# Optimization experiments

Hardware: AMD Instinct MI355X
Metric: run time of the kernel (lower is better)

Reference implementation:

```python
import jax, jax.numpy as jnp
import numpy as np

ES = 256
NUM_SPECIES, NUM_ABILITIES, NUM_ITEMS, NUM_MOVES = 1026, 300, 500, 920
NUM_ITEM_EFFECTS, NUM_GENDERS, NUM_STATUS, NUM_VOLATILE_STATUS = 16, 3, 8, 105
B, N, F = 8192, 12, 42
# feature layout (flat int32 vector per entity)
(SPECIES, ABILITY, ITEM, ITEM_EFFECT, GENDER, STATUS, BEING_CALLED_BACK, TRAPPED,
 NEWLY_SWITCHED, TOXIC_TURNS, SLEEP_TURNS, FAINTED, ACTIVE, SIDE, LEVEL, HP, MAXHP) = range(17)
BOOST0, VOL0, MOVEID0, MOVEPP0 = 17, 24, 33, 37  # 7 boosts, 9 volatile words, 4 moves, 4 pp

DENSE_DIMS = [("hp", 10), ("level", 7), ("active", 2), ("onehot", 32), ("boosts", 7),
              ("volatiles", NUM_VOLATILE_STATUS), ("item", ES + NUM_ITEM_EFFECTS),
              ("side", 2), ("moves", ES + 6)]

def _bits(x, world_dim):
    # binary-scale embedding: bit decomposition of an int feature
    nb = (world_dim - 1).bit_length()
    mask = jnp.asarray(1 << np.arange(nb), dtype=jnp.int32)
    return ((x[..., None] & mask) != 0).astype(jnp.float32)

def setup_inputs() -> dict:
    key = jax.random.key(0)
    ks = jax.random.split(key, 32)
    s = 0.02
    inp = {"entities": jax.random.randint(ks[0], (B, N, F), 0, 2, dtype=jnp.int32)}
    inp["embed_species"] = jax.random.normal(ks[1], (NUM_SPECIES, ES), jnp.float32) * s
    inp["embed_ability"] = jax.random.normal(ks[2], (NUM_ABILITIES, ES), jnp.float32) * s
    inp["embed_item"] = jax.random.normal(ks[3], (NUM_ITEMS, ES), jnp.float32) * s
    inp["embed_moves"] = jax.random.normal(ks[4], (NUM_MOVES, ES), jnp.float32) * s
    for i, (name, din) in enumerate(DENSE_DIMS):
        inp[f"{name}_W"] = jax.random.normal(ks[5 + i], (din, ES), jnp.float32) * s
        inp[f"{name}_b"] = jnp.zeros((ES,), jnp.float32)
    return inp

def _forward(entities, embed_species, embed_ability, embed_item, embed_moves,
             hp_W, hp_b, level_W, level_b, active_W, active_b, onehot_W, onehot_b,
             boosts_W, boosts_b, volatiles_W, volatiles_b, item_W, item_b,
             side_W, side_b, moves_W, moves_b):
    e = entities
    oh = jax.nn.one_hot
    dense = lambda x, W, b: x @ W + b
    hp = e[..., HP].astype(jnp.float32)
    maxhp = jnp.clip(e[..., MAXHP], 1).astype(jnp.float32)
    hp_ratio = jnp.clip(hp / maxhp, 0.0, 1.0)                      # (B,N)
    hp_token = jnp.floor(1023.0 * hp_ratio).astype(jnp.int32)
    boolean_code = jnp.concatenate([
        hp_ratio[..., None], oh(e[..., GENDER], NUM_GENDERS), oh(e[..., STATUS], NUM_STATUS),
        oh(e[..., BEING_CALLED_BACK], 2), oh(e[..., TRAPPED], 2), oh(e[..., NEWLY_SWITCHED], 2),
        oh(e[..., TOXIC_TURNS], 8), oh(e[..., SLEEP_TURNS], 4), oh(e[..., FAINTED], 2)], axis=-1)  # (B,N,32)
    item_onehot = jnp.concatenate([embed_item[e[..., ITEM]], oh(e[..., ITEM_EFFECT], NUM_ITEM_EFFECTS)], axis=-1)
    boosts = e[..., BOOST0:VOL0].astype(jnp.float32) / 2.0          # (B,N,7)
    vol = e[..., VOL0:VOL0 + 9]
    vbits = (vol[..., None] & jnp.arange(16)) > 0                   # (B,N,9,16)
    vol_oh = vbits.reshape(*vol.shape[:-1], 144)[..., :NUM_VOLATILE_STATUS].astype(jnp.float32)
    moveset = jnp.concatenate([embed_moves[e[..., MOVEID0:MOVEPP0]],
                               _bits(e[..., MOVEPP0:MOVEPP0 + 4], 64)], axis=-1)  # (B,N,4,262)
    moves_out = jnp.einsum('bnmf,fd->bnd', moveset, moves_W) + 4.0 * moves_b      # sum of 4 Dense outputs
    emb = (dense(_bits(hp_token, 1024), hp_W, hp_b)
           + dense(_bits(e[..., LEVEL], 101), level_W, level_b)
           + dense(oh(e[..., ACTIVE], 2), active_W, active_b)
           + dense(boolean_code, onehot_W, onehot_b)
           + dense(boosts, boosts_W, boosts_b)
           + dense(vol_oh, volatiles_W, volatiles_b)
           + embed_species[e[..., SPECIES]]
           + embed_ability[e[..., ABILITY]]
           + dense(item_onehot, item_W, item_b)
           + dense(oh(e[..., SIDE], 2), side_W, side_b)
           + moves_out)
    return emb

def reference(entities, embed_species, embed_ability, embed_item, embed_moves,
              hp_W, hp_b, level_W, level_b, active_W, active_b, onehot_W, onehot_b,
              boosts_W, boosts_b, volatiles_W, volatiles_b, item_W, item_b,
              side_W, side_b, moves_W, moves_b):
    return _forward(entities, embed_species, embed_ability, embed_item, embed_moves,
                    hp_W, hp_b, level_W, level_b, active_W, active_b, onehot_W, onehot_b,
                    boosts_W, boosts_b, volatiles_W, volatiles_b, item_W, item_b,
                    side_W, side_b, moves_W, moves_b)
```

## Files before the change

kernel.cpp:

```cpp
#include <hip/hip_runtime.h>
#include <hip/hip_fp16.h>

#define ES 256
#define NFEAT 42
#define NENT (8192 * 12)

#define F_SPECIES 0
#define F_ABILITY 1
#define F_ITEM 2
#define F_ITEM_EFFECT 3
#define F_GENDER 4
#define F_STATUS 5
#define F_BCB 6
#define F_TRAPPED 7
#define F_NEWSW 8
#define F_TOXIC 9
#define F_SLEEP 10
#define F_FAINTED 11
#define F_ACTIVE 12
#define F_SIDE 13
#define F_LEVEL 14
#define F_HP 15
#define F_MAXHP 16
#define F_BOOST0 17
#define F_VOL0 24
#define F_MOVEID0 33
#define F_MOVEPP0 37

#define OFF_HP     0
#define OFF_LV     (OFF_HP + 1024*ES)
#define OFF_PP     (OFF_LV + 128*ES)
#define OFF_VP     (OFF_PP + 64*ES)
#define OFF_CA     (OFF_VP + 784*ES)
#define OFF_CB     (OFF_CA + 768*ES)
#define OFF_EI     (OFF_CB + 1024*ES)
#define OFF_EM     (OFF_EI + 500*ES)
#define OFF_SP     (OFF_EM + 920*ES)
#define OFF_AB     (OFF_SP + 1026*ES)
#define WS_HALVES  (OFF_AB + 300*ES)

typedef float vf4 __attribute__((ext_vector_type(4)));

__device__ __forceinline__ float4 ld4(const float* p) {
    return *reinterpret_cast<const float4*>(p);
}
__device__ __forceinline__ void st4(float* p, const float4 v) {
    *reinterpret_cast<float4*>(p) = v;
}
__device__ __forceinline__ void st4_nt(float* p, const float4 v) {
    vf4 t = {v.x, v.y, v.z, v.w};
    __builtin_nontemporal_store(t, reinterpret_cast<vf4*>(p));
}
__device__ __forceinline__ void add4(float4& a, const float4 b) {
    a.x += b.x; a.y += b.y; a.z += b.z; a.w += b.w;
}
__device__ __forceinline__ float4 sum4(const float4 a, const float4 b) {
    return make_float4(a.x + b.x, a.y + b.y, a.z + b.z, a.w + b.w);
}
__device__ __forceinline__ void fma4(float4& a, float s, const float4 b) {
    a.x += s * b.x; a.y += s * b.y; a.z += s * b.z; a.w += s * b.w;
}
__device__ __forceinline__ int sclamp(int x, int lo, int hi) {
    return x < lo ? lo : (x > hi ? hi : x);
}
__device__ __forceinline__ void st4h(__half* p, const float4 v) {
    __half2 a = __floats2half2_rn(v.x, v.y);
    __half2 b = __floats2half2_rn(v.z, v.w);
    uint2 u;
    u.x = *reinterpret_cast<unsigned*>(&a);
    u.y = *reinterpret_cast<unsigned*>(&b);
    *reinterpret_cast<uint2*>(p) = u;
}
__device__ __forceinline__ float4 ldh4(const __half* p) {
    uint2 u = *reinterpret_cast<const uint2*>(p);
    __half2 a = *reinterpret_cast<__half2*>(&u.x);
    __half2 b = *reinterpret_cast<__half2*>(&u.y);
    float2 fa = __half22float2(a), fb = __half22float2(b);
    return make_float4(fa.x, fa.y, fb.x, fb.y);
}

#define TB_HP0 0
#define TB_LV0 256
#define TB_PP0 288
#define TB_VP0 304
#define TB_CA0 500
#define TB_CB0 692
#define TB_EI0 948
#define TB_EM0 1073
#define TB_SP0 1303
#define TB_AB0 1560
#define TB_TOT 1635

__global__ __launch_bounds__(256) void k_tables(
    const float* __restrict__ sp_e, const float* __restrict__ ab_e,
    const float* __restrict__ item_e, const float* __restrict__ moves_e,
    const float* __restrict__ hp_W, const float* __restrict__ level_W,
    const float* __restrict__ moves_W, const float* __restrict__ vol_W,
    const float* __restrict__ item_W, const float* __restrict__ onehot_W,
    const float* __restrict__ active_W, const float* __restrict__ side_W,
    const float* __restrict__ hp_b, const float* __restrict__ level_b,
    const float* __restrict__ active_b, const float* __restrict__ onehot_b,
    const float* __restrict__ boosts_b, const float* __restrict__ vol_b,
    const float* __restrict__ item_b, const float* __restrict__ side_b,
    const float* __restrict__ moves_b,
    __half* __restrict__ wh) {
    __shared__ float4 se4[4][64];
    const int bid = blockIdx.x, tid = threadIdx.x;
    const int rl = tid >> 6, lane = tid & 63, d0 = lane * 4;
    float4 acc = make_float4(0.f, 0.f, 0.f, 0.f);

    if (bid < TB_LV0) {
        int v = (bid - TB_HP0) * 4 + rl;
        for (int b = 0; b < 10; ++b)
            if ((v >> b) & 1) add4(acc, ld4(hp_W + b * ES + d0));
        st4h(wh + OFF_HP + v * ES + d0, acc);
    } else if (bid < TB_PP0) {
        int v = (bid - TB_LV0) * 4 + rl;
        for (int b = 0; b < 7; ++b)
            if ((v >> b) & 1) add4(acc, ld4(level_W + b * ES + d0));
        st4h(wh + OFF_LV + v * ES + d0, acc);
    } else if (bid < TB_VP0) {
        int v = (bid - TB_PP0) * 4 + rl;
        for (int b = 0; b < 6; ++b)
            if ((v >> b) & 1) add4(acc, ld4(moves_W + (256 + b) * ES + d0));
        st4h(wh + OFF_PP + v * ES + d0, acc);
    } else if (bid < TB_CA0) {
        int v = (bid - TB_VP0) * 4 + rl;
        if (v < 768) {
            int t = v >> 8, pair = v & 255, a = pair >> 4, b = pair & 15;
            for (int j = 0; j < 16; ++j) {
                if (a & j) add4(acc, ld4(vol_W + (32 * t + j) * ES + d0));
                if (b & j) add4(acc, ld4(vol_W + (32 * t + 16 + j) * ES + d0));
            }
        } else {
            int a = v - 768;
            for (int j = 0; j < 9; ++j)
                if (a & j) add4(acc, ld4(vol_W + (96 + j) * ES + d0));
        }
        st4h(wh + OFF_VP + v * ES + d0, acc);
    } else if (bid < TB_CB0) {
        int idx = (bid - TB_CA0) * 4 + rl;
        int fa = idx & 1, ns = (idx >> 1) & 1, tr = (idx >> 2) & 1, bcb = (idx >> 3) & 1;
        int rest = idx >> 4, g = rest % 3, e = rest / 3;
        acc = sum4(sum4(ld4(item_W + (256 + e) * ES + d0), ld4(onehot_W + (1 + g) * ES + d0)),
                   sum4(ld4(onehot_W + (12 + bcb) * ES + d0), ld4(onehot_W + (14 + tr) * ES + d0)));
        add4(acc, sum4(ld4(onehot_W + (16 + ns) * ES + d0), ld4(onehot_W + (30 + fa) * ES + d0)));
        st4h(wh + OFF_CA + idx * ES + d0, acc);
    } else if (bid < TB_EI0) {
        int idx = (bid - TB_CB0) * 4 + rl;
        int sd = idx & 1, act = (idx >> 1) & 1, sl = (idx >> 2) & 3,
            tox = (idx >> 4) & 7, st = idx >> 7;
        acc = sum4(sum4(ld4(hp_b + d0), ld4(level_b + d0)),
                   sum4(ld4(active_b + d0), ld4(onehot_b + d0)));
        add4(acc, sum4(ld4(boosts_b + d0), ld4(vol_b + d0)));
        add4(acc, sum4(ld4(item_b + d0), ld4(side_b + d0)));
        fma4(acc, 4.0f, ld4(moves_b + d0));
        add4(acc, sum4(ld4(onehot_W + (4 + st) * ES + d0), ld4(onehot_W + (18 + tox) * ES + d0)));
        add4(acc, sum4(ld4(onehot_W + (26 + sl) * ES + d0),
                       sum4(ld4(active_W + act * ES + d0), ld4(side_W + sd * ES + d0))));
        st4h(wh + OFF_CB + idx * ES + d0, acc);
    } else if (bid < TB_SP0) {
        const float* E; const float* W; __half* o; int r0;
        if (bid < TB_EM0) { E = item_e;  W = item_W;  o = wh + OFF_EI; r0 = (bid - TB_EI0) * 4; }
        else              { E = moves_e; W = moves_W; o = wh + OFF_EM; r0 = (bid - TB_EM0) * 4; }
        se4[tid >> 6][tid & 63] = ld4(E + r0 * ES + tid * 4);
        __syncthreads();
#pragma unroll 4
        for (int k0 = 0; k0 < 64; ++k0) {
            float4 e4 = se4[rl][k0];
            fma4(acc, e4.x, ld4(W + (4 * k0 + 0) * ES + d0));
            fma4(acc, e4.y, ld4(W + (4 * k0 + 1) * ES + d0));
            fma4(acc, e4.z, ld4(W + (4 * k0 + 2) * ES + d0));
            fma4(acc, e4.w, ld4(W + (4 * k0 + 3) * ES + d0));
        }
        st4h(o + (r0 + rl) * ES + d0, acc);
    } else if (bid < TB_AB0) {
        int r = (bid - TB_SP0) * 4 + rl;
        if (r < 1026) st4h(wh + OFF_SP + r * ES + d0, ld4(sp_e + r * ES + d0));
    } else {
        int r = (bid - TB_AB0) * 4 + rl;
        st4h(wh + OFF_AB + r * ES + d0, ld4(ab_e + r * ES + d0));
    }
}


__global__ __launch_bounds__(256) void k_main(
    const int* __restrict__ ent,
    const float* __restrict__ onehotW, const float* __restrict__ boostsW,
    const __half* __restrict__ wh,
    float* __restrict__ out) {
    __shared__ float lds[8 * ES];
    {
        int t = threadIdx.x;
        int row = t >> 5, col = (t & 31) * 8;
        const float* src = (row < 7) ? (boostsW + row * ES + col) : (onehotW + col);
        st4(&lds[row * ES + col], ld4(src));
        st4(&lds[row * ES + col + 4], ld4(src + 4));
    }
    __syncthreads();

    const int lane = threadIdx.x & 63;
    const int went = __builtin_amdgcn_readfirstlane((blockIdx.x * 256 + threadIdx.x) >> 6);
    const int d0 = lane * 4;

    int fv = __builtin_nontemporal_load(ent + went * NFEAT + (lane < NFEAT ? lane : 0));
#define RL(i) __builtin_amdgcn_readlane(fv, (i))

    const __half* Hp = wh + OFF_HP;
    const __half* Lv = wh + OFF_LV;
    const __half* Pp = wh + OFF_PP;
    const __half* VP = wh + OFF_VP;
    const __half* CA = wh + OFF_CA;
    const __half* CB = wh + OFF_CB;
    const __half* EI = wh + OFF_EI;
    const __half* EM = wh + OFF_EM;
    const __half* SP = wh + OFF_SP;
    const __half* AB = wh + OFF_AB;

    const int iB = ((((RL(F_STATUS) & 7) * 8 + (RL(F_TOXIC) & 7)) * 4 + (RL(F_SLEEP) & 3)) * 2 +
                    (RL(F_ACTIVE) & 1)) * 2 + (RL(F_SIDE) & 1);
    const int iA = (((((RL(F_ITEM_EFFECT) & 15) * 3 + sclamp(RL(F_GENDER), 0, 2)) * 2 +
                      (RL(F_BCB) & 1)) * 2 + (RL(F_TRAPPED) & 1)) * 2 +
                    (RL(F_NEWSW) & 1)) * 2 + (RL(F_FAINTED) & 1);
    const int iSP = sclamp(RL(F_SPECIES), 0, 1025);
    const int iAB = sclamp(RL(F_ABILITY), 0, 299);
    const int iIT = sclamp(RL(F_ITEM), 0, 499);
    const float hp = (float)RL(F_HP);
    int mh = RL(F_MAXHP); if (mh < 1) mh = 1;
    const float ratio = fminf(fmaxf(hp / (float)mh, 0.f), 1.f);
    const int tok = __builtin_amdgcn_readfirstlane((int)floorf(1023.f * ratio));
    const int iLV = RL(F_LEVEL) & 127;
    const int b0 = RL(F_BOOST0 + 0), b1 = RL(F_BOOST0 + 1), b2 = RL(F_BOOST0 + 2),
              b3 = RL(F_BOOST0 + 3), b4 = RL(F_BOOST0 + 4), b5 = RL(F_BOOST0 + 5),
              b6 = RL(F_BOOST0 + 6);
    const int vp0 = ((RL(F_VOL0 + 0) & 15) << 4) | (RL(F_VOL0 + 1) & 15);
    const int vp1 = ((RL(F_VOL0 + 2) & 15) << 4) | (RL(F_VOL0 + 3) & 15);
    const int vp2 = ((RL(F_VOL0 + 4) & 15) << 4) | (RL(F_VOL0 + 5) & 15);
    const int v6  = RL(F_VOL0 + 6) & 15;
    const int m0 = sclamp(RL(F_MOVEID0 + 0), 0, 919), m1 = sclamp(RL(F_MOVEID0 + 1), 0, 919),
              m2 = sclamp(RL(F_MOVEID0 + 2), 0, 919), m3 = sclamp(RL(F_MOVEID0 + 3), 0, 919);
    const int p0 = RL(F_MOVEPP0 + 0) & 63, p1 = RL(F_MOVEPP0 + 1) & 63,
              p2 = RL(F_MOVEPP0 + 2) & 63, p3 = RL(F_MOVEPP0 + 3) & 63;
#undef RL

    const float4 xCB = ldh4(CB + iB * ES + d0);
    const float4 xCA = ldh4(CA + iA * ES + d0);
    const float4 xSP = ldh4(SP + iSP * ES + d0);
    const float4 xAB = ldh4(AB + iAB * ES + d0);
    const float4 xIT = ldh4(EI + iIT * ES + d0);
    const float4 xHP = ldh4(Hp + tok * ES + d0);
    const float4 xLV = ldh4(Lv + iLV * ES + d0);
    const float4 xV0 = ldh4(VP + (0 * 256 + vp0) * ES + d0);
    const float4 xV1 = ldh4(VP + (1 * 256 + vp1) * ES + d0);
    const float4 xV2 = ldh4(VP + (2 * 256 + vp2) * ES + d0);
    const float4 xV6 = ldh4(VP + (768 + v6) * ES + d0);
    const float4 xP0 = ldh4(Pp + p0 * ES + d0);
    const float4 xP1 = ldh4(Pp + p1 * ES + d0);
    const float4 xP2 = ldh4(Pp + p2 * ES + d0);
    const float4 xP3 = ldh4(Pp + p3 * ES + d0);
    const float4 xE0 = ldh4(EM + m0 * ES + d0);
    const float4 xE1 = ldh4(EM + m1 * ES + d0);
    const float4 xE2 = ldh4(EM + m2 * ES + d0);
    const float4 xE3 = ldh4(EM + m3 * ES + d0);

    float4 s0 = sum4(sum4(xCB, xCA), sum4(xSP, xAB));
    float4 s1 = sum4(sum4(xIT, xHP), sum4(xLV, xV6));
    float4 s2 = sum4(sum4(xV0, xV1), sum4(xV2, xP0));
    float4 s3 = sum4(sum4(xE0, xE1), sum4(xE2, xE3));
    float4 s4 = sum4(sum4(xP1, xP2), xP3);
    float4 acc = sum4(sum4(s0, s1), sum4(s2, s3));
    add4(acc, s4);

    fma4(acc, ratio, ld4(&lds[7 * ES + d0]));
    fma4(acc, 0.5f * (float)b0, ld4(&lds[0 * ES + d0]));
    fma4(acc, 0.5f * (float)b1, ld4(&lds[1 * ES + d0]));
    fma4(acc, 0.5f * (float)b2, ld4(&lds[2 * ES + d0]));
    fma4(acc, 0.5f * (float)b3, ld4(&lds[3 * ES + d0]));
    fma4(acc, 0.5f * (float)b4, ld4(&lds[4 * ES + d0]));
    fma4(acc, 0.5f * (float)b5, ld4(&lds[5 * ES + d0]));
    fma4(acc, 0.5f * (float)b6, ld4(&lds[6 * ES + d0]));

    st4_nt(out + went * ES + d0, acc);
}


extern "C" void kernel_launch(void* const* d_in, const int* in_sizes, int n_in,
                              void* d_out, int out_size, void* d_ws, size_t ws_size,
                              hipStream_t stream) {
    const int*   entities = (const int*)  d_in[0];
    const float* sp       = (const float*)d_in[1];
    const float* ab       = (const float*)d_in[2];
    const float* item_e   = (const float*)d_in[3];
    const float* moves_e  = (const float*)d_in[4];
    const float* hp_W     = (const float*)d_in[5];
    const float* hp_b     = (const float*)d_in[6];
    const float* level_W  = (const float*)d_in[7];
    const float* level_b  = (const float*)d_in[8];
    const float* active_W = (const float*)d_in[9];
    const float* active_b = (const float*)d_in[10];
    const float* onehot_W = (const float*)d_in[11];
    const float* onehot_b = (const float*)d_in[12];
    const float* boosts_W = (const float*)d_in[13];
    const float* boosts_b = (const float*)d_in[14];
    const float* vol_W    = (const float*)d_in[15];
    const float* vol_b    = (const float*)d_in[16];
    const float* item_W   = (const float*)d_in[17];
    const float* item_b   = (const float*)d_in[18];
    const float* side_W   = (const float*)d_in[19];
    const float* side_b   = (const float*)d_in[20];
    const float* moves_W  = (const float*)d_in[21];
    const float* moves_b  = (const float*)d_in[22];

    __half* wh  = (__half*)d_ws;
    float*  out = (float*)d_out;

    k_tables<<<TB_TOT, 256, 0, stream>>>(
        sp, ab, item_e, moves_e, hp_W, level_W, moves_W, vol_W,
        item_W, onehot_W, active_W, side_W,
        hp_b, level_b, active_b, onehot_b, boosts_b,
        vol_b, item_b, side_b, moves_b, wh);

    k_main<<<NENT / 4, 256, 0, stream>>>(entities, onehot_W, boosts_W, wh, out);
}
```

Before: 232.9 us.

## Process two entities per wavefront with 16-byte half loads per lane

Each 64-lane wavefront now handles two entities, one per half-wave. Each lane loads 8 halfs (uint4) per table row instead of 4, and the grid is halved. The feature vectors for both entities are read with two loads and readlane, and per-lane selects pick the indices. This halves wavefront count and widens the memory accesses to reduce instruction and launch overhead. In exchange the table gathers become per-lane divergent addresses (vector rather than scalar-uniform indices), and more registers are used per lane.

Result: faster. 212.0 us (-9.0%).

```diff
diff --git a/kernel.cpp b/kernel.cpp
--- a/kernel.cpp
+++ b/kernel.cpp
@@ -70,13 +70,6 @@
     u.x = *reinterpret_cast<unsigned*>(&a);
     u.y = *reinterpret_cast<unsigned*>(&b);
     *reinterpret_cast<uint2*>(p) = u;
-}
-__device__ __forceinline__ float4 ldh4(const __half* p) {
-    uint2 u = *reinterpret_cast<const uint2*>(p);
-    __half2 a = *reinterpret_cast<__half2*>(&u.x);
-    __half2 b = *reinterpret_cast<__half2*>(&u.y);
-    float2 fa = __half22float2(a), fb = __half22float2(b);
-    return make_float4(fa.x, fa.y, fb.x, fb.y);
 }
 
 #define TB_HP0 0
@@ -199,12 +192,20 @@
     }
     __syncthreads();
 
-    const int lane = threadIdx.x & 63;
-    const int went = __builtin_amdgcn_readfirstlane((blockIdx.x * 256 + threadIdx.x) >> 6);
-    const int d0 = lane * 4;
-
-    int fv = __builtin_nontemporal_load(ent + went * NFEAT + (lane < NFEAT ? lane : 0));
-#define RL(i) __builtin_amdgcn_readlane(fv, (i))
+    const int lane  = threadIdx.x & 63;
+    const int wpair = __builtin_amdgcn_readfirstlane((blockIdx.x * 256 + threadIdx.x) >> 6);
+    const int entA  = wpair * 2;
+    const int e     = lane >> 5;
+    const int sub   = lane & 31;
+    const int sub8  = sub * 8;
+    const int base  = entA * NFEAT;
+
+    const int fv  = __builtin_nontemporal_load(ent + base + lane);
+    const int fv2 = __builtin_nontemporal_load(ent + base + 52 + sub);
+
+#define RLA(i) __builtin_amdgcn_readlane(fv, (i))
+#define RLB(i) ((i) < 22 ? __builtin_amdgcn_readlane(fv, 42 + (i)) \
+                         : __builtin_amdgcn_readlane(fv2, (i) - 10))
 
     const __half* Hp = wh + OFF_HP;
     const __half* Lv = wh + OFF_LV;
@@ -217,70 +218,99 @@
     const __half* SP = wh + OFF_SP;
     const __half* AB = wh + OFF_AB;
 
-    const int iB = ((((RL(F_STATUS) & 7) * 8 + (RL(F_TOXIC) & 7)) * 4 + (RL(F_SLEEP) & 3)) * 2 +
-                    (RL(F_ACTIVE) & 1)) * 2 + (RL(F_SIDE) & 1);
-    const int iA = (((((RL(F_ITEM_EFFECT) & 15) * 3 + sclamp(RL(F_GENDER), 0, 2)) * 2 +
-                      (RL(F_BCB) & 1)) * 2 + (RL(F_TRAPPED) & 1)) * 2 +
-                    (RL(F_NEWSW) & 1)) * 2 + (RL(F_FAINTED) & 1);
-    const int iSP = sclamp(RL(F_SPECIES), 0, 1025);
-    const int iAB = sclamp(RL(F_ABILITY), 0, 299);
-    const int iIT = sclamp(RL(F_ITEM), 0, 499);
-    const float hp = (float)RL(F_HP);
-    int mh = RL(F_MAXHP); if (mh < 1) mh = 1;
-    const float ratio = fminf(fmaxf(hp / (float)mh, 0.f), 1.f);
-    const int tok = __builtin_amdgcn_readfirstlane((int)floorf(1023.f * ratio));
-    const int iLV = RL(F_LEVEL) & 127;
-    const int b0 = RL(F_BOOST0 + 0), b1 = RL(F_BOOST0 + 1), b2 = RL(F_BOOST0 + 2),
-              b3 = RL(F_BOOST0 + 3), b4 = RL(F_BOOST0 + 4), b5 = RL(F_BOOST0 + 5),
-              b6 = RL(F_BOOST0 + 6);
-    const int vp0 = ((RL(F_VOL0 + 0) & 15) << 4) | (RL(F_VOL0 + 1) & 15);
-    const int vp1 = ((RL(F_VOL0 + 2) & 15) << 4) | (RL(F_VOL0 + 3) & 15);
-    const int vp2 = ((RL(F_VOL0 + 4) & 15) << 4) | (RL(F_VOL0 + 5) & 15);
-    const int v6  = RL(F_VOL0 + 6) & 15;
-    const int m0 = sclamp(RL(F_MOVEID0 + 0), 0, 919), m1 = sclamp(RL(F_MOVEID0 + 1), 0, 919),
-              m2 = sclamp(RL(F_MOVEID0 + 2), 0, 919), m3 = sclamp(RL(F_MOVEID0 + 3), 0, 919);
-    const int p0 = RL(F_MOVEPP0 + 0) & 63, p1 = RL(F_MOVEPP0 + 1) & 63,
-              p2 = RL(F_MOVEPP0 + 2) & 63, p3 = RL(F_MOVEPP0 + 3) & 63;
-#undef RL
-
-    const float4 xCB = ldh4(CB + iB * ES + d0);
-    const float4 xCA = ldh4(CA + iA * ES + d0);
-    const float4 xSP = ldh4(SP + iSP * ES + d0);
-    const float4 xAB = ldh4(AB + iAB * ES + d0);
-    const float4 xIT = ldh4(EI + iIT * ES + d0);
-    const float4 xHP = ldh4(Hp + tok * ES + d0);
-    const float4 xLV = ldh4(Lv + iLV * ES + d0);
-    const float4 xV0 = ldh4(VP + (0 * 256 + vp0) * ES + d0);
-    const float4 xV1 = ldh4(VP + (1 * 256 + vp1) * ES + d0);
-    const float4 xV2 = ldh4(VP + (2 * 256 + vp2) * ES + d0);
-    const float4 xV6 = ldh4(VP + (768 + v6) * ES + d0);
-    const float4 xP0 = ldh4(Pp + p0 * ES + d0);
-    const float4 xP1 = ldh4(Pp + p1 * ES + d0);
-    const float4 xP2 = ldh4(Pp + p2 * ES + d0);
-    const float4 xP3 = ldh4(Pp + p3 * ES + d0);
-    const float4 xE0 = ldh4(EM + m0 * ES + d0);
-    const float4 xE1 = ldh4(EM + m1 * ES + d0);
-    const float4 xE2 = ldh4(EM + m2 * ES + d0);
-    const float4 xE3 = ldh4(EM + m3 * ES + d0);
-
-    float4 s0 = sum4(sum4(xCB, xCA), sum4(xSP, xAB));
-    float4 s1 = sum4(sum4(xIT, xHP), sum4(xLV, xV6));
-    float4 s2 = sum4(sum4(xV0, xV1), sum4(xV2, xP0));
-    float4 s3 = sum4(sum4(xE0, xE1), sum4(xE2, xE3));
-    float4 s4 = sum4(sum4(xP1, xP2), xP3);
-    float4 acc = sum4(sum4(s0, s1), sum4(s2, s3));
-    add4(acc, s4);
-
-    fma4(acc, ratio, ld4(&lds[7 * ES + d0]));
-    fma4(acc, 0.5f * (float)b0, ld4(&lds[0 * ES + d0]));
-    fma4(acc, 0.5f * (float)b1, ld4(&lds[1 * ES + d0]));
-    fma4(acc, 0.5f * (float)b2, ld4(&lds[2 * ES + d0]));
-    fma4(acc, 0.5f * (float)b3, ld4(&lds[3 * ES + d0]));
-    fma4(acc, 0.5f * (float)b4, ld4(&lds[4 * ES + d0]));
-    fma4(acc, 0.5f * (float)b5, ld4(&lds[5 * ES + d0]));
-    fma4(acc, 0.5f * (float)b6, ld4(&lds[6 * ES + d0]));
-
-    st4_nt(out + went * ES + d0, acc);
+#define IDX_BLOCK(RL, S) \
+    const int iCB##S = ((((RL(F_STATUS) & 7) * 8 + (RL(F_TOXIC) & 7)) * 4 + (RL(F_SLEEP) & 3)) * 2 + \
+                        (RL(F_ACTIVE) & 1)) * 2 + (RL(F_SIDE) & 1); \
+    const int iCA##S = (((((RL(F_ITEM_EFFECT) & 15) * 3 + sclamp(RL(F_GENDER), 0, 2)) * 2 + \
+                          (RL(F_BCB) & 1)) * 2 + (RL(F_TRAPPED) & 1)) * 2 + \
+                        (RL(F_NEWSW) & 1)) * 2 + (RL(F_FAINTED) & 1); \
+    const int iSP##S = sclamp(RL(F_SPECIES), 0, 1025); \
+    const int iAB##S = sclamp(RL(F_ABILITY), 0, 299); \
+    const int iIT##S = sclamp(RL(F_ITEM), 0, 499); \
+    float hpv##S = (float)RL(F_HP); \
+    int mh##S = RL(F_MAXHP); if (mh##S < 1) mh##S = 1; \
+    const float ratio##S = fminf(fmaxf(hpv##S / (float)mh##S, 0.f), 1.f); \
+    const int tok##S = (int)floorf(1023.f * ratio##S); \
+    const int iLV##S = RL(F_LEVEL) & 127; \
+    const int vp0##S = ((RL(F_VOL0 + 0) & 15) << 4) | (RL(F_VOL0 + 1) & 15); \
+    const int vp1##S = ((RL(F_VOL0 + 2) & 15) << 4) | (RL(F_VOL0 + 3) & 15); \
+    const int vp2##S = ((RL(F_VOL0 + 4) & 15) << 4) | (RL(F_VOL0 + 5) & 15); \
+    const int v6##S  = RL(F_VOL0 + 6) & 15; \
+    const int m0##S = sclamp(RL(F_MOVEID0 + 0), 0, 919), m1##S = sclamp(RL(F_MOVEID0 + 1), 0, 919), \
+              m2##S = sclamp(RL(F_MOVEID0 + 2), 0, 919), m3##S = sclamp(RL(F_MOVEID0 + 3), 0, 919); \
+    const int p0##S = RL(F_MOVEPP0 + 0) & 63, p1##S = RL(F_MOVEPP0 + 1) & 63, \
+              p2##S = RL(F_MOVEPP0 + 2) & 63, p3##S = RL(F_MOVEPP0 + 3) & 63; \
+    const float b0##S = (float)RL(F_BOOST0 + 0), b1##S = (float)RL(F_BOOST0 + 1), \
+                b2##S = (float)RL(F_BOOST0 + 2), b3##S = (float)RL(F_BOOST0 + 3), \
+                b4##S = (float)RL(F_BOOST0 + 4), b5##S = (float)RL(F_BOOST0 + 5), \
+                b6##S = (float)RL(F_BOOST0 + 6);
+
+    IDX_BLOCK(RLA, A)
+    IDX_BLOCK(RLB, B)
+#undef RLA
+#undef RLB
+#undef IDX_BLOCK
+
+#define SEL(x) (e ? x##B : x##A)
+    const int jCB = SEL(iCB), jCA = SEL(iCA), jSP = SEL(iSP), jAB = SEL(iAB), jIT = SEL(iIT);
+    const int jHP = SEL(tok), jLV = SEL(iLV);
+    const int jV0 = SEL(vp0), jV1 = SEL(vp1), jV2 = SEL(vp2), jV6 = SEL(v6);
+    const int jP0 = SEL(p0), jP1 = SEL(p1), jP2 = SEL(p2), jP3 = SEL(p3);
+    const int jM0 = SEL(m0), jM1 = SEL(m1), jM2 = SEL(m2), jM3 = SEL(m3);
+    const float ratio = SEL(ratio);
+    const float s0v = 0.5f * SEL(b0), s1v = 0.5f * SEL(b1), s2v = 0.5f * SEL(b2),
+                s3v = 0.5f * SEL(b3), s4v = 0.5f * SEL(b4), s5v = 0.5f * SEL(b5),
+                s6v = 0.5f * SEL(b6);
+#undef SEL
+
+#define LD8(n, tab, idx) const uint4 n = *reinterpret_cast<const uint4*>((tab) + (idx) * ES + sub8)
+    LD8(uCB, CB, jCB);
+    LD8(uCA, CA, jCA);
+    LD8(uSP, SP, jSP);
+    LD8(uAB, AB, jAB);
+    LD8(uIT, EI, jIT);
+    LD8(uHP, Hp, jHP);
+    LD8(uLV, Lv, jLV);
+    LD8(uV0, VP, 0 * 256 + jV0);
+    LD8(uV1, VP, 1 * 256 + jV1);
+    LD8(uV2, VP, 2 * 256 + jV2);
+    LD8(uV6, VP, 768 + jV6);
+    LD8(uP0, Pp, jP0);
+    LD8(uP1, Pp, jP1);
+    LD8(uP2, Pp, jP2);
+    LD8(uP3, Pp, jP3);
+    LD8(uE0, EM, jM0);
+    LD8(uE1, EM, jM1);
+    LD8(uE2, EM, jM2);
+    LD8(uE3, EM, jM3);
+#undef LD8
+
+    float4 a0 = make_float4(0.f, 0.f, 0.f, 0.f);
+    float4 a1 = make_float4(0.f, 0.f, 0.f, 0.f);
+#define ACC(u) { \
+    __half2 h; float2 f; \
+    h = *reinterpret_cast<const __half2*>(&u.x); f = __half22float2(h); a0.x += f.x; a0.y += f.y; \
+    h = *reinterpret_cast<const __half2*>(&u.y); f = __half22float2(h); a0.z += f.x; a0.w += f.y; \
+    h = *reinterpret_cast<const __half2*>(&u.z); f = __half22float2(h); a1.x += f.x; a1.y += f.y; \
+    h = *reinterpret_cast<const __half2*>(&u.w); f = __half22float2(h); a1.z += f.x; a1.w += f.y; }
+    ACC(uCB) ACC(uCA) ACC(uSP) ACC(uAB) ACC(uIT) ACC(uHP) ACC(uLV)
+    ACC(uV0) ACC(uV1) ACC(uV2) ACC(uV6)
+    ACC(uP0) ACC(uP1) ACC(uP2) ACC(uP3)
+    ACC(uE0) ACC(uE1) ACC(uE2) ACC(uE3)
+#undef ACC
+
+    fma4(a0, ratio, ld4(&lds[7 * ES + sub8]));     fma4(a1, ratio, ld4(&lds[7 * ES + sub8 + 4]));
+    fma4(a0, s0v, ld4(&lds[0 * ES + sub8]));       fma4(a1, s0v, ld4(&lds[0 * ES + sub8 + 4]));
+    fma4(a0, s1v, ld4(&lds[1 * ES + sub8]));       fma4(a1, s1v, ld4(&lds[1 * ES + sub8 + 4]));
+    fma4(a0, s2v, ld4(&lds[2 * ES + sub8]));       fma4(a1, s2v, ld4(&lds[2 * ES + sub8 + 4]));
+    fma4(a0, s3v, ld4(&lds[3 * ES + sub8]));       fma4(a1, s3v, ld4(&lds[3 * ES + sub8 + 4]));
+    fma4(a0, s4v, ld4(&lds[4 * ES + sub8]));       fma4(a1, s4v, ld4(&lds[4 * ES + sub8 + 4]));
+    fma4(a0, s5v, ld4(&lds[5 * ES + sub8]));       fma4(a1, s5v, ld4(&lds[5 * ES + sub8 + 4]));
+    fma4(a0, s6v, ld4(&lds[6 * ES + sub8]));       fma4(a1, s6v, ld4(&lds[6 * ES + sub8 + 4]));
+
+    float* op = out + (entA + e) * ES + sub8;
+    st4_nt(op, a0);
+    st4_nt(op + 4, a1);
 }
 
 
@@ -320,5 +350,5 @@
         hp_b, level_b, active_b, onehot_b, boosts_b,
         vol_b, item_b, side_b, moves_b, wh);
 
-    k_main<<<NENT / 4, 256, 0, stream>>>(entities, onehot_W, boosts_W, wh, out);
-}
+    k_main<<<NENT / 8, 256, 0, stream>>>(entities, onehot_W, boosts_W, wh, out);
+}
```
